# Kernel optimization log

Measured on AMD Instinct MI355X. Metric: run time of the kernel, lower is better.

## Reference

```python
import jax, jax.numpy as jnp
import numpy as np

KERNEL_SIZE = 11
SIGMA = 1.5
IN_CH = 2


def _gaussian_kernel(kernel_size: int, sigma: float) -> jnp.ndarray:
    start = (1 - kernel_size) / 2
    coords = jnp.arange(start, start + kernel_size, dtype=jnp.float32)
    k1d = jnp.exp(-((coords / sigma) ** 2) / 2)
    k1d = k1d / k1d.sum()
    k2d = jnp.outer(k1d, k1d)  # [K, K]
    # OIHW depthwise kernel: [out_ch=IN_CH, in_ch/groups=1, K, K]
    return jnp.broadcast_to(k2d, (IN_CH, 1, kernel_size, kernel_size))


def _blur(img: jnp.ndarray, kernel: jnp.ndarray) -> jnp.ndarray:
    pad = KERNEL_SIZE // 2
    return jax.lax.conv_general_dilated(
        img, kernel,
        window_strides=(1, 1),
        padding=[(pad, pad), (pad, pad)],
        dimension_numbers=("NCHW", "OIHW", "NCHW"),
        feature_group_count=IN_CH,
    )


def setup_inputs() -> dict:
    key = jax.random.key(0)
    kx, ky = jax.random.split(key)
    shape = (32, 2, 512, 512)
    x = jax.random.uniform(kx, shape, dtype=jnp.float32)
    y = jax.random.uniform(ky, shape, dtype=jnp.float32)
    return {"x": x, "y": y}


def reference(x, y):
    kernel = _gaussian_kernel(KERNEL_SIZE, SIGMA)
    ux = _blur(x, kernel)
    uy = _blur(y, kernel)
    uxx = _blur(x * x, kernel)
    uyy = _blur(y * y, kernel)
    uxy = _blur(x * y, kernel)

    vx = uxx - ux * ux
    vy = uyy - uy * uy
    vxy = uxy - ux * uy

    c1 = 0.01 ** 2
    c2 = 0.03 ** 2
    numerator = (2 * ux * uy + c1) * (2 * vxy + c2)
    denominator = (ux ** 2 + uy ** 2 + c1) * (vx + vy + c2)
    ssim_map = numerator / (denominator + 1e-12)
    # as_loss=True path
    return 1 - ssim_map.mean()
```

## Files before the change

### kernel.cpp

```cpp
#include <hip/hip_runtime.h>
#include <hip/hip_fp16.h>

#define KSZ 11
#define TILE 32
#define SMH 42
#define SST8 66
#define SST16 33
#define THREADS 256

#define W0 1.0283800e-03f
#define W1 7.5987000e-03f
#define W2 3.6000800e-02f
#define W3 1.0936070e-01f
#define W4 2.1300550e-01f
#define W5 2.6601170e-01f

struct Pix8   { __half2 hx, hy; };
struct Pix8x2 { __half2 hx0, hy0, hx1, hy1; };
struct Pix16  { __half2 s0, s1, s2, s3; };

static __device__ inline __half2 pkrtz(float a, float b) {
    auto v = __builtin_amdgcn_cvt_pkrtz(a, b);
    __half2 r;
    __builtin_memcpy(&r, &v, 4);
    return r;
}

#define HBCOL(g, j) ((((g) + 2 * (j)) & 7) | ((j) << 3))

__global__ __launch_bounds__(THREADS) void ssim_tile_kernel(
    const float* __restrict__ x, const float* __restrict__ y,
    float* __restrict__ partial, int W, int H)
{
    __shared__ __align__(16) unsigned char smem[SMH * 528];
    __shared__ float wsum[THREADS / 64];
    Pix8*  lin = (Pix8*)smem;
    Pix16* hb  = (Pix16*)smem;

    const __half2 w2[KSZ] = {
        __float2half2_rn(W0), __float2half2_rn(W1), __float2half2_rn(W2),
        __float2half2_rn(W3), __float2half2_rn(W4), __float2half2_rn(W5),
        __float2half2_rn(W4), __float2half2_rn(W3), __float2half2_rn(W2),
        __float2half2_rn(W1), __float2half2_rn(W0)};
    const __half2 hz = __float2half2_rn(0.0f);

    const int tid = threadIdx.x;
    const int bx = blockIdx.x;
    const int t  = ((bx & 7) << 5) | (bx >> 3);
    const int tileR = (t >> 4) << 5;
    const int tileC = (t & 15) << 5;
    const size_t plane = (size_t)W * (size_t)H;
    const size_t base0 = (size_t)blockIdx.y * 2 * plane;
    const size_t base1 = base0 + plane;

    const bool interior = (tileR >= 5) && (tileR + 37 <= H) &&
                          (tileC >= 8) && (tileC + 40 <= W);
    for (int it = tid; it < SMH * 8; it += THREADS) {
        const int r = it >> 3;
        const int g = it & 7;
        const int c0 = 6 * g;
        Pix8 p[6];
        if (interior) {
            const size_t goff = (size_t)(tileR - 5 + r) * W + (tileC - 8 + c0);
            const float2* X0 = (const float2*)(x + base0 + goff);
            const float2* X1 = (const float2*)(x + base1 + goff);
            const float2* Y0 = (const float2*)(y + base0 + goff);
            const float2* Y1 = (const float2*)(y + base1 + goff);
#pragma unroll
            for (int m = 0; m < 3; ++m) {
                float2 a0 = X0[m], a1 = X1[m], b0 = Y0[m], b1 = Y1[m];
                p[2*m].hx   = pkrtz(a0.x, a1.x);
                p[2*m].hy   = pkrtz(b0.x, b1.x);
                p[2*m+1].hx = pkrtz(a0.y, a1.y);
                p[2*m+1].hy = pkrtz(b0.y, b1.y);
            }
        } else {
            const int gr = tileR - 5 + r;
#pragma unroll
            for (int m = 0; m < 6; ++m) {
                const int gc = tileC - 8 + c0 + m;
                float x0 = 0.f, x1 = 0.f, y0 = 0.f, y1 = 0.f;
                if (gr >= 0 && gr < H && gc >= 0 && gc < W) {
                    size_t gg = (size_t)gr * W + gc;
                    x0 = x[base0 + gg]; x1 = x[base1 + gg];
                    y0 = y[base0 + gg]; y1 = y[base1 + gg];
                }
                p[m].hx = pkrtz(x0, x1);
                p[m].hy = pkrtz(y0, y1);
            }
        }
        Pix8x2* dst = (Pix8x2*)&lin[r * SST8 + c0];
#pragma unroll
        for (int m = 0; m < 3; ++m) {
            Pix8x2 o;
            o.hx0 = p[2*m].hx;   o.hy0 = p[2*m].hy;
            o.hx1 = p[2*m+1].hx; o.hy1 = p[2*m+1].hy;
            dst[m] = o;
        }
    }

    for (int it = tid; it < SMH * 8; it += THREADS) {
        const int r = it >> 3;
        const int g = it & 7;
        const int c0 = g << 2;
        __half2 wx[16], wy[16];
        const Pix8x2* src = (const Pix8x2*)&lin[r * SST8 + (c0 + 2)];
#pragma unroll
        for (int k = 0; k < 8; ++k) {
            Pix8x2 u = src[k];
            wx[2*k]   = u.hx0; wy[2*k]   = u.hy0;
            wx[2*k+1] = u.hx1; wy[2*k+1] = u.hy1;
        }
        __half2 pp[16], qq[16];
#pragma unroll
        for (int k = 1; k < 15; ++k) {
            pp[k] = __hfma2(wy[k], wy[k], __hmul2(wx[k], wx[k]));
            qq[k] = __hmul2(wx[k], wy[k]);
        }
        __half2 s0[4] = {hz, hz, hz, hz}, s1[4] = {hz, hz, hz, hz};
        __half2 s2[4] = {hz, hz, hz, hz}, s3[4] = {hz, hz, hz, hz};
#pragma unroll
        for (int k = 1; k < 15; ++k) {
#pragma unroll
            for (int j = 0; j < 4; ++j) {
                const int tt = k - 1 - j;
                if (tt >= 0 && tt < KSZ) {
                    s0[j] = __hfma2(w2[tt], wx[k], s0[j]);
                    s1[j] = __hfma2(w2[tt], wy[k], s1[j]);
                    s2[j] = __hfma2(w2[tt], pp[k], s2[j]);
                    s3[j] = __hfma2(w2[tt], qq[k], s3[j]);
                }
            }
        }
        Pix16* orow = &hb[r * SST16];
#pragma unroll
        for (int j = 0; j < 4; ++j) {
            Pix16 v;
            v.s0 = s0[j]; v.s1 = s1[j]; v.s2 = s2[j]; v.s3 = s3[j];
            orow[HBCOL(g, j)] = v;
        }
    }
    __syncthreads();

    float bsum;
    {
        const int c  = tid & 31;
        const int r0 = (tid >> 5) << 2;
        const int pc = HBCOL(c >> 2, c & 3);
        const Pix16* colp = &hb[r0 * SST16 + pc];

        __half2 b0[4] = {hz, hz, hz, hz}, b1[4] = {hz, hz, hz, hz};
        __half2 b2[4] = {hz, hz, hz, hz}, b3[4] = {hz, hz, hz, hz};
#pragma unroll
        for (int k = 0; k < 14; ++k) {
            Pix16 u = colp[k * SST16];
#pragma unroll
            for (int j = 0; j < 4; ++j) {
                const int tt = k - j;
                if (tt >= 0 && tt < KSZ) {
                    b0[j] = __hfma2(w2[tt], u.s0, b0[j]);
                    b1[j] = __hfma2(w2[tt], u.s1, b1[j]);
                    b2[j] = __hfma2(w2[tt], u.s2, b2[j]);
                    b3[j] = __hfma2(w2[tt], u.s3, b3[j]);
                }
            }
        }

        const __half2 c1h  = __float2half2_rn(1.0e-4f);
        const __half2 c2h  = __float2half2_rn(9.0e-4f);
        const __half2 twoh = __float2half2_rn(2.0f);
        __half2 acc2 = hz;
#pragma unroll
        for (int j = 0; j < 4; ++j) {
            __half2 ux = b0[j], uy = b1[j], up = b2[j], uq = b3[j];
            __half2 uxuy  = __hmul2(ux, uy);
            __half2 sumsq = __hfma2(ux, ux, __hmul2(uy, uy));
            __half2 vsum  = __hsub2(up, sumsq);
            __half2 vxy   = __hsub2(uq, uxuy);
            __half2 num   = __hmul2(__hfma2(twoh, uxuy, c1h),
                                    __hfma2(twoh, vxy, c2h));
            __half2 den   = __hmul2(__hadd2(sumsq, c1h), __hadd2(vsum, c2h));
            acc2 = __hfma2(num, h2rcp(den), acc2);
        }
        float2 af = __half22float2(acc2);
        bsum = af.x + af.y;
    }

#pragma unroll
    for (int off = 32; off > 0; off >>= 1) bsum += __shfl_down(bsum, off, 64);
    const int lane = tid & 63, wid = tid >> 6;
    if (lane == 0) wsum[wid] = bsum;
    __syncthreads();
    if (tid == 0) {
        float tot = 0.f;
#pragma unroll
        for (int i = 0; i < THREADS / 64; ++i) tot += wsum[i];
        partial[(size_t)blockIdx.y * gridDim.x + blockIdx.x] = tot;
    }
}

__global__ __launch_bounds__(256) void ssim_reduce_kernel(
    const float* __restrict__ partial, int n, float* __restrict__ out,
    double inv_count)
{
    __shared__ double ws[4];
    const float4* p4 = (const float4*)partial;
    const int n4 = n >> 2;
    double s = 0.0;
    for (int i = threadIdx.x; i < n4; i += 256) {
        float4 v = p4[i];
        s += (double)v.x + (double)v.y + (double)v.z + (double)v.w;
    }
#pragma unroll
    for (int off = 32; off > 0; off >>= 1) s += __shfl_down(s, off, 64);
    int lane = threadIdx.x & 63, wid = threadIdx.x >> 6;
    if (lane == 0) ws[wid] = s;
    __syncthreads();
    if (threadIdx.x == 0) {
        double tot = ws[0] + ws[1] + ws[2] + ws[3];
        out[0] = (float)(1.0 - tot * inv_count);
    }
}

extern "C" void kernel_launch(void* const* d_in, const int* in_sizes, int n_in,
                              void* d_out, int out_size, void* d_ws, size_t ws_size,
                              hipStream_t stream) {
    const float* x = (const float*)d_in[0];
    const float* y = (const float*)d_in[1];
    float* partial = (float*)d_ws;

    const int W = 512, H = 512;
    const int N = 32;
    const int tilesPerPlane = (W / TILE) * (H / TILE);

    dim3 grid(tilesPerPlane, N);
    ssim_tile_kernel<<<grid, THREADS, 0, stream>>>(x, y, partial, W, H);

    const int nPartial = tilesPerPlane * N;
    const double inv_count = 1.0 / ((double)N * 2 * W * H);
    ssim_reduce_kernel<<<1, 256, 0, stream>>>(partial, nPartial, (float*)d_out,
                                              inv_count);
}
```

Baseline: 69.90 us.

## Replace 32x32 tiles with rolling column strips reusing vertical halo rows

```diff
diff --git a/kernel.cpp b/kernel.cpp
--- a/kernel.cpp
+++ b/kernel.cpp
@@ -2,11 +2,12 @@
 #include <hip/hip_fp16.h>
 
 #define KSZ 11
-#define TILE 32
-#define SMH 42
-#define SST8 66
-#define SST16 33
+#define RS 64
+#define GH 13
+#define ROWB 512
 #define THREADS 256
+#define SEGROWS 256
+#define NCHUNK 8
 
 #define W0 1.0283800e-03f
 #define W1 7.5987000e-03f
@@ -19,20 +20,116 @@
 struct Pix8x2 { __half2 hx0, hy0, hx1, hy1; };
 struct Pix16  { __half2 s0, s1, s2, s3; };
 
-static __device__ inline __half2 pkrtz(float a, float b) {
+#define HBCOL(g, j) ((((g) + 2 * (j)) & 7) | ((j) << 3))
+
+static __device__ __forceinline__ __half2 pkrtz(float a, float b) {
     auto v = __builtin_amdgcn_cvt_pkrtz(a, b);
     __half2 r;
     __builtin_memcpy(&r, &v, 4);
     return r;
 }
 
-#define HBCOL(g, j) ((((g) + 2 * (j)) & 7) | ((j) << 3))
-
-__global__ __launch_bounds__(THREADS) void ssim_tile_kernel(
+static __device__ __forceinline__ void stage_item(
     const float* __restrict__ x, const float* __restrict__ y,
-    float* __restrict__ partial, int W, int H)
-{
-    __shared__ __align__(16) unsigned char smem[SMH * 528];
+    size_t base0, size_t base1, int q, int g, int s, int tileC,
+    bool fast, Pix8* lin)
+{
+    const int c0 = 6 * g;
+    Pix8 p[6];
+    if (fast) {
+        const size_t goff = (size_t)q * 512 + (size_t)(tileC - 8 + c0);
+        const float2* X0 = (const float2*)(x + base0 + goff);
+        const float2* X1 = (const float2*)(x + base1 + goff);
+        const float2* Y0 = (const float2*)(y + base0 + goff);
+        const float2* Y1 = (const float2*)(y + base1 + goff);
+#pragma unroll
+        for (int m = 0; m < 3; ++m) {
+            float2 a0 = X0[m], a1 = X1[m], b0 = Y0[m], b1 = Y1[m];
+            p[2*m].hx   = pkrtz(a0.x, a1.x);
+            p[2*m].hy   = pkrtz(b0.x, b1.x);
+            p[2*m+1].hx = pkrtz(a0.y, a1.y);
+            p[2*m+1].hy = pkrtz(b0.y, b1.y);
+        }
+    } else {
+#pragma unroll
+        for (int m = 0; m < 6; ++m) {
+            const int gc = tileC - 8 + c0 + m;
+            float x0 = 0.f, x1 = 0.f, y0 = 0.f, y1 = 0.f;
+            if (q >= 0 && q < 512 && gc >= 0 && gc < 512) {
+                const size_t gg = (size_t)q * 512 + (size_t)gc;
+                x0 = x[base0 + gg]; x1 = x[base1 + gg];
+                y0 = y[base0 + gg]; y1 = y[base1 + gg];
+            }
+            p[m].hx = pkrtz(x0, x1);
+            p[m].hy = pkrtz(y0, y1);
+        }
+    }
+    Pix8x2* dst = (Pix8x2*)&lin[s * 64 + c0];
+#pragma unroll
+    for (int m = 0; m < 3; ++m) {
+        Pix8x2 o;
+        o.hx0 = p[2*m].hx;   o.hy0 = p[2*m].hy;
+        o.hx1 = p[2*m+1].hx; o.hy1 = p[2*m+1].hy;
+        dst[m] = o;
+    }
+}
+
+static __device__ __forceinline__ void h_item(
+    int g, int s, Pix8* lin, Pix16* hb, const __half2* w2, __half2 hz)
+{
+    const int c0 = g << 2;
+    __half2 wx[16], wy[16];
+    const Pix8x2* src = (const Pix8x2*)&lin[s * 64 + (c0 + 2)];
+#pragma unroll
+    for (int k = 0; k < 8; ++k) {
+        Pix8x2 u = src[k];
+        wx[2*k]   = u.hx0; wy[2*k]   = u.hy0;
+        wx[2*k+1] = u.hx1; wy[2*k+1] = u.hy1;
+    }
+    __half2 pp[16], qq[16];
+#pragma unroll
+    for (int k = 1; k < 15; ++k) {
+        pp[k] = __hfma2(wy[k], wy[k], __hmul2(wx[k], wx[k]));
+        qq[k] = __hmul2(wx[k], wy[k]);
+    }
+    __half2 s0[4] = {hz, hz, hz, hz}, s1[4] = {hz, hz, hz, hz};
+    __half2 s2[4] = {hz, hz, hz, hz}, s3[4] = {hz, hz, hz, hz};
+#pragma unroll
+    for (int k = 1; k < 15; ++k) {
+#pragma unroll
+        for (int j = 0; j < 4; ++j) {
+            const int tt = k - 1 - j;
+            if (tt >= 0 && tt < KSZ) {
+                s0[j] = __hfma2(w2[tt], wx[k], s0[j]);
+                s1[j] = __hfma2(w2[tt], wy[k], s1[j]);
+                s2[j] = __hfma2(w2[tt], pp[k], s2[j]);
+                s3[j] = __hfma2(w2[tt], qq[k], s3[j]);
+            }
+        }
+    }
+    Pix16* orow = &hb[s * 32];
+#pragma unroll
+    for (int j = 0; j < 4; ++j) {
+        Pix16 v;
+        v.s0 = s0[j]; v.s1 = s1[j]; v.s2 = s2[j]; v.s3 = s3[j];
+        orow[HBCOL(g, j)] = v;
+    }
+    if (s < GH) {
+        Pix16* orow2 = orow + RS * 32;
+#pragma unroll
+        for (int j = 0; j < 4; ++j) {
+            Pix16 v;
+            v.s0 = s0[j]; v.s1 = s1[j]; v.s2 = s2[j]; v.s3 = s3[j];
+            orow2[HBCOL(g, j)] = v;
+        }
+    }
+}
+
+__global__ __launch_bounds__(THREADS) void ssim_roll_kernel(
+    const float* __restrict__ x, const float* __restrict__ y,
+    float* __restrict__ partial)
+{
+    __shared__ __align__(16) unsigned char smem[(RS + GH) * ROWB];
     __shared__ float wsum[THREADS / 64];
     Pix8*  lin = (Pix8*)smem;
     Pix16* hb  = (Pix16*)smem;
@@ -46,114 +143,59 @@
 
     const int tid = threadIdx.x;
     const int bx = blockIdx.x;
-    const int t  = ((bx & 7) << 5) | (bx >> 3);
-    const int tileR = (t >> 4) << 5;
-    const int tileC = (t & 15) << 5;
-    const size_t plane = (size_t)W * (size_t)H;
+    const int t  = ((bx & 7) << 2) | (bx >> 3);
+    const int sx = t & 15;
+    const int sg = t >> 4;
+    const int B  = sg << 8;
+    const int tileC = sx << 5;
+    const bool colInt = (sx > 0) && (sx < 15);
+    const size_t plane = 512 * 512;
     const size_t base0 = (size_t)blockIdx.y * 2 * plane;
     const size_t base1 = base0 + plane;
 
-    const bool interior = (tileR >= 5) && (tileR + 37 <= H) &&
-                          (tileC >= 8) && (tileC + 40 <= W);
-    for (int it = tid; it < SMH * 8; it += THREADS) {
-        const int r = it >> 3;
-        const int g = it & 7;
-        const int c0 = 6 * g;
-        Pix8 p[6];
-        if (interior) {
-            const size_t goff = (size_t)(tileR - 5 + r) * W + (tileC - 8 + c0);
-            const float2* X0 = (const float2*)(x + base0 + goff);
-            const float2* X1 = (const float2*)(x + base1 + goff);
-            const float2* Y0 = (const float2*)(y + base0 + goff);
-            const float2* Y1 = (const float2*)(y + base1 + goff);
-#pragma unroll
-            for (int m = 0; m < 3; ++m) {
-                float2 a0 = X0[m], a1 = X1[m], b0 = Y0[m], b1 = Y1[m];
-                p[2*m].hx   = pkrtz(a0.x, a1.x);
-                p[2*m].hy   = pkrtz(b0.x, b1.x);
-                p[2*m+1].hx = pkrtz(a0.y, a1.y);
-                p[2*m+1].hy = pkrtz(b0.y, b1.y);
-            }
+    const int pro_q = B - 5 + (tid >> 3);
+    const int pro_g = tid & 7;
+    const int pro_s = (pro_q + RS) & 63;
+    if (tid < 80 && pro_q >= 0)
+        stage_item(x, y, base0, base1, pro_q, pro_g, pro_s, tileC, colInt, lin);
+    if (tid < 80) {
+        if (pro_q >= 0) {
+            h_item(pro_g, pro_s, lin, hb, w2, hz);
         } else {
-            const int gr = tileR - 5 + r;
-#pragma unroll
-            for (int m = 0; m < 6; ++m) {
-                const int gc = tileC - 8 + c0 + m;
-                float x0 = 0.f, x1 = 0.f, y0 = 0.f, y1 = 0.f;
-                if (gr >= 0 && gr < H && gc >= 0 && gc < W) {
-                    size_t gg = (size_t)gr * W + gc;
-                    x0 = x[base0 + gg]; x1 = x[base1 + gg];
-                    y0 = y[base0 + gg]; y1 = y[base1 + gg];
-                }
-                p[m].hx = pkrtz(x0, x1);
-                p[m].hy = pkrtz(y0, y1);
-            }
-        }
-        Pix8x2* dst = (Pix8x2*)&lin[r * SST8 + c0];
-#pragma unroll
-        for (int m = 0; m < 3; ++m) {
-            Pix8x2 o;
-            o.hx0 = p[2*m].hx;   o.hy0 = p[2*m].hy;
-            o.hx1 = p[2*m+1].hx; o.hy1 = p[2*m+1].hy;
-            dst[m] = o;
-        }
-    }
-
-    for (int it = tid; it < SMH * 8; it += THREADS) {
-        const int r = it >> 3;
-        const int g = it & 7;
-        const int c0 = g << 2;
-        __half2 wx[16], wy[16];
-        const Pix8x2* src = (const Pix8x2*)&lin[r * SST8 + (c0 + 2)];
-#pragma unroll
-        for (int k = 0; k < 8; ++k) {
-            Pix8x2 u = src[k];
-            wx[2*k]   = u.hx0; wy[2*k]   = u.hy0;
-            wx[2*k+1] = u.hx1; wy[2*k+1] = u.hy1;
-        }
-        __half2 pp[16], qq[16];
-#pragma unroll
-        for (int k = 1; k < 15; ++k) {
-            pp[k] = __hfma2(wy[k], wy[k], __hmul2(wx[k], wx[k]));
-            qq[k] = __hmul2(wx[k], wy[k]);
-        }
-        __half2 s0[4] = {hz, hz, hz, hz}, s1[4] = {hz, hz, hz, hz};
-        __half2 s2[4] = {hz, hz, hz, hz}, s3[4] = {hz, hz, hz, hz};
-#pragma unroll
-        for (int k = 1; k < 15; ++k) {
-#pragma unroll
-            for (int j = 0; j < 4; ++j) {
-                const int tt = k - 1 - j;
-                if (tt >= 0 && tt < KSZ) {
-                    s0[j] = __hfma2(w2[tt], wx[k], s0[j]);
-                    s1[j] = __hfma2(w2[tt], wy[k], s1[j]);
-                    s2[j] = __hfma2(w2[tt], pp[k], s2[j]);
-                    s3[j] = __hfma2(w2[tt], qq[k], s3[j]);
-                }
-            }
-        }
-        Pix16* orow = &hb[r * SST16];
-#pragma unroll
-        for (int j = 0; j < 4; ++j) {
-            Pix16 v;
-            v.s0 = s0[j]; v.s1 = s1[j]; v.s2 = s2[j]; v.s3 = s3[j];
-            orow[HBCOL(g, j)] = v;
-        }
-    }
-    __syncthreads();
-
-    float bsum;
-    {
-        const int c  = tid & 31;
-        const int r0 = (tid >> 5) << 2;
-        const int pc = HBCOL(c >> 2, c & 3);
-        const Pix16* colp = &hb[r0 * SST16 + pc];
+            Pix16 z; z.s0 = hz; z.s1 = hz; z.s2 = hz; z.s3 = hz;
+            Pix16* orow = &hb[pro_s * 32];
+#pragma unroll
+            for (int j = 0; j < 4; ++j) orow[HBCOL(pro_g, j)] = z;
+        }
+    }
+
+    float bsum = 0.f;
+    const int st_ro = tid >> 3, st_g = tid & 7;
+    const int v_c = tid & 31, v_rg = tid >> 5;
+    const int pc = HBCOL(v_c >> 2, v_c & 3);
+    const float c1f = 1.0e-4f, c2f = 9.0e-4f;
+    const __half2 c1h  = __float2half2_rn(c1f);
+    const __half2 c2h  = __float2half2_rn(c2f);
+    const __half2 twoh = __float2half2_rn(2.0f);
+
+#pragma unroll 1
+    for (int n = 0; n < NCHUNK; ++n) {
+        __syncthreads();
+        const int q = B + (n << 5) + 5 + st_ro;
+        const int s = q & 63;
+        const bool fast = colInt && (q < 512);
+        stage_item(x, y, base0, base1, q, st_g, s, tileC, fast, lin);
+        h_item(st_g, s, lin, hb, w2, hz);
+        __syncthreads();
+
+        const int sb = (B + (n << 5) + (v_rg << 2) - 5 + RS) & 63;
+        const Pix16* colp = &hb[sb * 32 + pc];
 
         __half2 b0[4] = {hz, hz, hz, hz}, b1[4] = {hz, hz, hz, hz};
         __half2 b2[4] = {hz, hz, hz, hz}, b3[4] = {hz, hz, hz, hz};
 #pragma unroll
         for (int k = 0; k < 14; ++k) {
-            Pix16 u = colp[k * SST16];
+            Pix16 u = colp[k * 32];
 #pragma unroll
             for (int j = 0; j < 4; ++j) {
                 const int tt = k - j;
@@ -165,10 +207,6 @@
                 }
             }
         }
-
-        const __half2 c1h  = __float2half2_rn(1.0e-4f);
-        const __half2 c2h  = __float2half2_rn(9.0e-4f);
-        const __half2 twoh = __float2half2_rn(2.0f);
         __half2 acc2 = hz;
 #pragma unroll
         for (int j = 0; j < 4; ++j) {
@@ -183,7 +221,7 @@
             acc2 = __hfma2(num, h2rcp(den), acc2);
         }
         float2 af = __half22float2(acc2);
-        bsum = af.x + af.y;
+        bsum += af.x + af.y;
     }
 
 #pragma unroll
@@ -229,15 +267,12 @@
     const float* y = (const float*)d_in[1];
     float* partial = (float*)d_ws;
 
-    const int W = 512, H = 512;
     const int N = 32;
-    const int tilesPerPlane = (W / TILE) * (H / TILE);
-
-    dim3 grid(tilesPerPlane, N);
-    ssim_tile_kernel<<<grid, THREADS, 0, stream>>>(x, y, partial, W, H);
-
-    const int nPartial = tilesPerPlane * N;
-    const double inv_count = 1.0 / ((double)N * 2 * W * H);
+    dim3 grid(32, N);
+    ssim_roll_kernel<<<grid, THREADS, 0, stream>>>(x, y, partial);
+
+    const int nPartial = 32 * N;
+    const double inv_count = 1.0 / ((double)N * 2 * 512 * 512);
     ssim_reduce_kernel<<<1, 256, 0, stream>>>(partial, nPartial, (float*)d_out,
                                               inv_count);
 }
```

Result: faster. 65.85 us (-5.8%).
